# Kernel optimization log

Hardware: AMD Instinct MI355X
Metric: run time of the kernel (lower is better)

The kernel has to match this reference:

```python
import jax, jax.numpy as jnp
import numpy as np

B, P = 8, 768
S = 36                 # sample_points (also deformable offset pairs)
C_IN, C_ADJ = 64, 72   # prior_feat_channels -> adjusted channels
D, G = 512, 4          # fc_hidden_dim, num_groups (= attention heads)
N_OFFSETS, N_STRIPS, DEG = 72, 71, 3


def _bilinear(img, x, y):
    """img: [B,H,W,C]; x,y: [B,N] pixel coords. Bilinear sample, zeros outside."""
    H, W = img.shape[1], img.shape[2]
    x0 = jnp.floor(x); y0 = jnp.floor(y)
    x0i = x0.astype(jnp.int32); y0i = y0.astype(jnp.int32)
    wx1 = x - x0; wy1 = y - y0

    def corner(xi, yi, w):
        valid = (xi >= 0) & (xi < W) & (yi >= 0) & (yi < H)
        xc = jnp.clip(xi, 0, W - 1); yc = jnp.clip(yi, 0, H - 1)
        vals = jax.vmap(lambda f, yy, xx: f[yy, xx])(img, yc, xc)  # [B,N,C]
        return vals * (w * valid)[..., None]

    return (corner(x0i, y0i, (1 - wx1) * (1 - wy1))
            + corner(x0i + 1, y0i, wx1 * (1 - wy1))
            + corner(x0i, y0i + 1, (1 - wx1) * wy1)
            + corner(x0i + 1, y0i + 1, wx1 * wy1))


def _resize_ac(img, Ht, Wt):
    """Bilinear resize with align_corners=True. img: [B,H,W,C]."""
    Bsz, H, W, _ = img.shape
    gy, gx = jnp.meshgrid(jnp.linspace(0.0, H - 1.0, Ht),
                          jnp.linspace(0.0, W - 1.0, Wt), indexing='ij')
    xf = jnp.broadcast_to(gx.reshape(-1), (Bsz, Ht * Wt))
    yf = jnp.broadcast_to(gy.reshape(-1), (Bsz, Ht * Wt))
    return _bilinear(img, xf, yf).reshape(Bsz, Ht, Wt, -1)


def setup_inputs():
    ks = jax.random.split(jax.random.key(0), 32)
    r = lambda i, shp, s=1.0: jax.random.normal(ks[i], shp, dtype=jnp.float32) * s
    z = lambda shp: jnp.zeros(shp, jnp.float32)
    return {
        'feat0': r(0, (B, C_IN, 40, 100)),
        'feat1': r(1, (B, C_IN, 20, 50)),
        'feat2': r(2, (B, C_IN, 10, 25)),
        'priors': jax.random.uniform(ks[3], (B, P, 4 + N_OFFSETS), dtype=jnp.float32) * N_STRIPS,
        'ca_w': r(4, (C_ADJ, C_IN), 0.125), 'ca_b': z((C_ADJ,)),
        'off_w': r(5, (2 * S, C_ADJ), 0.01), 'off_b': r(6, (2 * S,), 0.01),
        'dp_w': r(7, (C_ADJ, C_ADJ), 0.167), 'dp_b': z((C_ADJ,)),
        'z_emb': r(8, (S,), 0.3) + 1.0,
        'gf_w': r(9, (D, S // G, C_ADJ), 0.02), 'gf_b': z((D,)),
        'wq': r(10, (D, D), 0.044), 'bq': z((D,)),
        'wk': r(11, (D, D), 0.044), 'bk': z((D,)),
        'wv': r(12, (D, D), 0.044), 'bv': z((D,)),
        'wo': r(13, (D, D), 0.044), 'bo': z((D,)),
        'cf_w1': r(14, (2 * D, D), 0.044), 'cf_b1': z((2 * D,)),
        'cf_w2': r(15, (D, 2 * D), 0.031), 'cf_b2': z((D,)),
        'cls_w1': r(16, (D, D), 0.044), 'cls_b1': z((D,)),
        'cls_w2': r(17, (2, D), 0.001), 'cls_b2': z((2,)),
        'reg_w1': r(18, (D, D), 0.044), 'reg_b1': z((D,)),
        'p_w1': r(19, (2 * D, D), 0.044), 'p_b1': z((2 * D,)),
        'p_w2': r(20, (DEG + 1, 2 * D), 0.031), 'p_b2': z((DEG + 1,)),
        'b_scale': jnp.ones((1,), jnp.float32), 'b_bias': z((1,)),
    }


def reference(feat0, feat1, feat2, priors, ca_w, ca_b, off_w, off_b, dp_w, dp_b,
              z_emb, gf_w, gf_b, wq, bq, wk, bk, wv, bv, wo, bo,
              cf_w1, cf_b1, cf_w2, cf_b2, cls_w1, cls_b1, cls_w2, cls_b2,
              reg_w1, reg_b1, p_w1, p_b1, p_w2, p_b2, b_scale, b_bias):
    f32 = jnp.float32
    lin = lambda x, w, b: x @ w.T + b

    # ---- prior sampling grid (CLRNet-style) ----
    sx_idx = jnp.floor(jnp.linspace(0.0, 1.0, S) * N_STRIPS).astype(jnp.int32)
    pf_ys = jnp.flip(1.0 - sx_idx.astype(f32) / N_STRIPS)            # [S]
    pf_xs = priors[..., 4 + sx_idx][:, :, ::-1]                       # [B,P,S]
    gx = jnp.clip(pf_xs / N_STRIPS, 0.0, 1.0) * 2.0 - 1.0            # [-1,1]
    gy = jnp.broadcast_to(pf_ys * 2.0 - 1.0, gx.shape)

    # ---- channel adjust (1x1 conv) per level, channels-last ----
    adj = lambda f: jnp.einsum('bchw,oc->bhwo', f, ca_w) + ca_b
    feats = [adj(feat0), adj(feat1), adj(feat2)]                      # [B,H,W,C_ADJ]
    offs0 = jnp.einsum('bhwc,oc->bhwo', feats[0], off_w) + off_b     # [B,H0,W0,2S]

    # ---- deformable multi-level sampling: per (prior, point) gather + 1x1 proj ----
    sidx = jnp.arange(S)
    levels = []
    for l, fl in enumerate(feats):
        Hl, Wl = fl.shape[1], fl.shape[2]
        offs = offs0 if l == 0 else _resize_ac(offs0, Hl, Wl)
        px = (gx + 1.0) * 0.5 * (Wl - 1)
        py = (gy + 1.0) * 0.5 * (Hl - 1)
        ov = _bilinear(offs, px.reshape(B, -1), py.reshape(B, -1)).reshape(B, P, S, S, 2)
        dyx = ov[:, :, sidx, sidx, :]                                 # offset pair s for point s
        sxp = (px + dyx[..., 1]).reshape(B, -1)
        syp = (py + dyx[..., 0]).reshape(B, -1)
        smp = _bilinear(fl, sxp, syp).reshape(B, P, S, C_ADJ)
        levels.append(smp @ dp_w.T + dp_b)
    feat_all = jnp.stack(levels)                                      # [3,B,P,S,C]

    # ---- z-embedding soft level selection ----
    zw = jax.nn.softmax(-(z_emb[:, None] - jnp.arange(3, dtype=f32)) ** 2 / 2.0, axis=-1)  # [S,3]
    feature = jnp.einsum('lbpsc,sl->bpsc', feat_all, zw)

    # ---- grouped gather Conv1d(S -> D, kernel=C_ADJ, groups=G) ----
    xg = feature.reshape(B * P, G, S // G, C_ADJ)
    wg = gf_w.reshape(G, D // G, S // G, C_ADJ)
    feature = (jnp.einsum('ngik,goik->ngo', xg, wg).reshape(B * P, D) + gf_b).reshape(B, P, D)

    # ---- multi-head self-attention over priors + channel MLP residual ----
    dh = D // G
    q = lin(feature, wq, bq).reshape(B, P, G, dh).transpose(0, 2, 1, 3)
    k = lin(feature, wk, bk).reshape(B, P, G, dh).transpose(0, 2, 1, 3)
    v = lin(feature, wv, bv).reshape(B, P, G, dh).transpose(0, 2, 1, 3)
    attn = jax.nn.softmax(jnp.einsum('bgqd,bgkd->bgqk', q, k) / float(np.sqrt(dh)), axis=-1)
    res = jnp.einsum('bgqk,bgkd->bgqd', attn, v).transpose(0, 2, 1, 3).reshape(B, P, D)
    res = lin(res, wo, bo)
    feature = feature + lin(jax.nn.relu(lin(res, cf_w1, cf_b1)), cf_w2, cf_b2)

    # ---- heads ----
    fc = feature.reshape(B * P, D)
    cls_logits = lin(jax.nn.relu(lin(fc, cls_w1, cls_b1)), cls_w2, cls_b2).reshape(B, P, 2)
    reg = jax.nn.relu(lin(fc, reg_w1, reg_b1)).reshape(B, P, D)
    coeffs = lin(jax.nn.relu(lin(reg, p_w1, p_b1)), p_w2, p_b2)       # [B,P,DEG+1]
    coeffs = jnp.concatenate([coeffs[..., :2], coeffs[..., 2:] * b_scale + b_bias], axis=-1)
    ys = jnp.linspace(0.0, 1.0, N_OFFSETS)
    basis = jnp.stack([ys ** i for i in range(DEG + 1)], axis=1)      # [N_OFFSETS, DEG+1]
    xs_pred = jax.nn.sigmoid(jnp.einsum('bnd,od->bno', coeffs, basis))
    return jnp.concatenate([cls_logits, coeffs, xs_pred], axis=-1)    # [B,P,78]
```

## Files before the change

kernel.cpp:

```cpp
#include <hip/hip_runtime.h>
#include <hip/hip_bf16.h>
#include <math.h>

#define BB 8
#define PP 768
#define NPRI 76
#define SS 36
#define CIN 64
#define CADJ 72
#define DD 512

#define H0 40
#define W0 100
#define H1 20
#define W1 50
#define H2 10
#define W2 25

typedef __attribute__((ext_vector_type(8))) short bf16x8;
typedef __attribute__((ext_vector_type(4))) short bf16x4;
typedef __attribute__((ext_vector_type(4))) float f32x4;
#define MFMA_BF16 __builtin_amdgcn_mfma_f32_16x16x32_bf16

typedef const __attribute__((address_space(1))) unsigned int* gas_t;
typedef __attribute__((address_space(3))) unsigned int* las_t;

__device__ __forceinline__ __hip_bfloat16 to_bf16(float v) { return __float2bfloat16(v); }
__device__ __forceinline__ float bf2f(__hip_bfloat16 v) { return __bfloat162float(v); }
__device__ __forceinline__ short to_bf16s(float v) {
    __hip_bfloat16 h = __float2bfloat16(v);
    return *reinterpret_cast<short*>(&h);
}
__device__ __forceinline__ float bfs2f(short s) {
    union { unsigned u; float f; } cv;
    cv.u = ((unsigned)(unsigned short)s) << 16;
    return cv.f;
}

__device__ __forceinline__ float bsample(const float* __restrict__ img, int H, int W,
                                         int C, int c, float x, float y)
{
    float x0f = floorf(x), y0f = floorf(y);
    int x0 = (int)x0f, y0 = (int)y0f;
    float wx1 = x - x0f, wy1 = y - y0f;
    float wx0 = 1.0f - wx1, wy0 = 1.0f - wy1;
    int xc0 = min(max(x0, 0), W - 1);
    int xc1 = min(max(x0 + 1, 0), W - 1);
    int yc0 = min(max(y0, 0), H - 1);
    int yc1 = min(max(y0 + 1, 0), H - 1);
    bool vx0 = (x0 >= 0) && (x0 < W);
    bool vx1 = (x0 + 1 >= 0) && (x0 + 1 < W);
    bool vy0 = (y0 >= 0) && (y0 < H);
    bool vy1 = (y0 + 1 >= 0) && (y0 + 1 < H);
    float w00 = (vx0 && vy0) ? wx0 * wy0 : 0.0f;
    float w01 = (vx1 && vy0) ? wx1 * wy0 : 0.0f;
    float w10 = (vx0 && vy1) ? wx0 * wy1 : 0.0f;
    float w11 = (vx1 && vy1) ? wx1 * wy1 : 0.0f;
    return w00 * img[((size_t)yc0 * W + xc0) * C + c]
         + w01 * img[((size_t)yc0 * W + xc1) * C + c]
         + w10 * img[((size_t)yc1 * W + xc0) * C + c]
         + w11 * img[((size_t)yc1 * W + xc1) * C + c];
}

__device__ __forceinline__ void cast4(__hip_bfloat16* dst, const float* src, long i)
{
    const float4 v = *(const float4*)(src + i * 4);
    bf16x4 pk;
    pk[0] = to_bf16s(v.x); pk[1] = to_bf16s(v.y);
    pk[2] = to_bf16s(v.z); pk[3] = to_bf16s(v.w);
    *(bf16x4*)(dst + i * 4) = pk;
}

__global__ __launch_bounds__(256) void k_wprep(
    const float* __restrict__ wq, const float* __restrict__ wk, const float* __restrict__ wv,
    const float* __restrict__ wo, const float* __restrict__ cf_w1, const float* __restrict__ cf_w2,
    const float* __restrict__ cls_w1, const float* __restrict__ reg_w1, const float* __restrict__ p_w1,
    const float* __restrict__ bq, const float* __restrict__ bk, const float* __restrict__ bv,
    const float* __restrict__ cls_b1, const float* __restrict__ reg_b1,
    const float* __restrict__ gf_w, const float* __restrict__ dp_w,
    const float* __restrict__ dp_b, const float* __restrict__ gf_b,
    __hip_bfloat16* __restrict__ wqkv, __hip_bfloat16* __restrict__ wo_bf,
    __hip_bfloat16* __restrict__ cf1_bf, __hip_bfloat16* __restrict__ cf2_bf,
    __hip_bfloat16* __restrict__ clsreg_bf, __hip_bfloat16* __restrict__ p1_bf,
    __hip_bfloat16* __restrict__ gfw2, float* __restrict__ b2,
    float* __restrict__ bqkv, float* __restrict__ bclsreg)
{
    __shared__ float dpS[CADJ][CADJ + 1];
    __shared__ float gfr[648];
    const int bid = blockIdx.x;
    const int tid = threadIdx.x;

    if (bid < 512) {
        const int o = bid;
        for (int i = tid; i < CADJ * CADJ; i += 256) dpS[i / CADJ][i % CADJ] = dp_w[i];
        for (int i = tid; i < 648; i += 256) gfr[i] = gf_w[(size_t)o * 648 + i];
        __syncthreads();
        for (int t = tid; t < 672; t += 256) {
            float acc = 0.0f;
            if (t < 648) {
                const int i = t / 72, m = t % 72;
                const float* gr = gfr + i * 72;
#pragma unroll 8
                for (int k = 0; k < 72; ++k) acc = fmaf(gr[k], dpS[k][m], acc);
            }
            gfw2[(size_t)o * 672 + t] = to_bf16(acc);
        }
        return;
    }
    if (bid < 514) {
        const int o = (bid - 512) * 256 + tid;
        if (o < DD) {
            const float* gr = gf_w + (size_t)o * 648;
            float acc = gf_b[o];
            for (int j = 0; j < 648; ++j) acc = fmaf(gr[j], dp_b[j % 72], acc);
            b2[o] = acc;
        }
        return;
    }
    if (bid < 3586) {
        long i = (long)(bid - 514) * 256 + tid;
        if (i < 65536) { cast4(wqkv, wq, i); return; }
        i -= 65536;
        if (i < 65536) { cast4(wqkv + 262144, wk, i); return; }
        i -= 65536;
        if (i < 65536) { cast4(wqkv + 524288, wv, i); return; }
        i -= 65536;
        if (i < 65536) { cast4(wo_bf, wo, i); return; }
        i -= 65536;
        if (i < 131072) { cast4(cf1_bf, cf_w1, i); return; }
        i -= 131072;
        if (i < 131072) { cast4(cf2_bf, cf_w2, i); return; }
        i -= 131072;
        if (i < 65536) { cast4(clsreg_bf, cls_w1, i); return; }
        i -= 65536;
        if (i < 65536) { cast4(clsreg_bf + 262144, reg_w1, i); return; }
        i -= 65536;
        if (i < 131072) { cast4(p1_bf, p_w1, i); return; }
        return;
    }
    for (int i = tid; i < 2560; i += 256) {
        if (i < 512) bqkv[i] = bq[i];
        else if (i < 1024) bqkv[i] = bk[i - 512];
        else if (i < 1536) bqkv[i] = bv[i - 1024];
        else if (i < 2048) bclsreg[i - 1536] = cls_b1[i - 1536];
        else bclsreg[i - 1536] = reg_b1[i - 2048];
    }
}

__global__ __launch_bounds__(256) void k_adjoff(
    const float* __restrict__ f, const float* __restrict__ caw, const float* __restrict__ cab,
    const float* __restrict__ offw, const float* __restrict__ offb,
    __hip_bfloat16* __restrict__ feout, float* __restrict__ offout, int HW, int do_off)
{
    __shared__ float inS[64][65];
    __shared__ float wS[72][64];
    __shared__ float owS[72][73];
    __shared__ float feS[64][73];
    __shared__ float cabS[72], obS[72];

    const int tid = threadIdx.x;
    const int b = blockIdx.y;
    const int pix0 = blockIdx.x * 64;
    const int cnt = min(64, HW - pix0);
    const int px = tid & 63, og = tid >> 6, o0 = og * 18;

    const float* fb = f + (size_t)b * CIN * HW + pix0;
    for (int i = tid; i < 72 * 64; i += 256) wS[i >> 6][i & 63] = caw[i];
    if (do_off)
        for (int i = tid; i < 72 * 72; i += 256) owS[i / 72][i % 72] = offw[i];
    if (tid < 72) { cabS[tid] = cab[tid]; obS[tid] = do_off ? offb[tid] : 0.f; }
    for (int i = tid; i < 64 * 64; i += 256) {
        const int c = i >> 6, p = i & 63;
        inS[c][p] = (p < cnt) ? fb[(size_t)c * HW + p] : 0.f;
    }
    __syncthreads();

    float acc[18];
#pragma unroll
    for (int j = 0; j < 18; ++j) acc[j] = cabS[o0 + j];
#pragma unroll 4
    for (int c = 0; c < 64; ++c) {
        const float v = inS[c][px];
#pragma unroll
        for (int j = 0; j < 18; ++j) acc[j] = fmaf(v, wS[o0 + j][c], acc[j]);
    }
#pragma unroll
    for (int j = 0; j < 18; ++j) feS[px][o0 + j] = acc[j];
    __syncthreads();

    __hip_bfloat16* feg = feout + ((size_t)b * HW + pix0) * CADJ;
    for (int i = tid; i < cnt * CADJ; i += 256) feg[i] = to_bf16(feS[i / CADJ][i % CADJ]);

    if (!do_off) return;

    float acc2[18];
#pragma unroll
    for (int j = 0; j < 18; ++j) acc2[j] = obS[o0 + j];
#pragma unroll 4
    for (int c = 0; c < 72; ++c) {
        const float v = feS[px][c];
#pragma unroll
        for (int j = 0; j < 18; ++j) acc2[j] = fmaf(v, owS[o0 + j][c], acc2[j]);
    }
    __syncthreads();
#pragma unroll
    for (int j = 0; j < 18; ++j) feS[px][o0 + j] = acc2[j];
    __syncthreads();
    float* ofg = offout + ((size_t)b * HW + pix0) * CADJ;
    for (int i = tid; i < cnt * CADJ; i += 256) ofg[i] = feS[i / CADJ][i % CADJ];
}

__global__ __launch_bounds__(256) void k_adjr12(
    const float* __restrict__ f1, const float* __restrict__ f2,
    const float* __restrict__ caw, const float* __restrict__ cab,
    __hip_bfloat16* __restrict__ fe1, __hip_bfloat16* __restrict__ fe2,
    const float* __restrict__ of0, float* __restrict__ of1, float* __restrict__ of2)
{
    const int blk = blockIdx.x;
    const int tid = threadIdx.x;

    if (blk < 160) {
        __shared__ float inS[64][65];
        __shared__ float wS[72][64];
        __shared__ float feS[64][73];
        __shared__ float cabS[72];

        const int bx = blk % 20;
        const int b = blk / 20;
        const float* f;
        __hip_bfloat16* fe;
        int HW, pix0;
        if (bx < 16) { f = f1; fe = fe1; HW = H1 * W1; pix0 = bx * 64; }
        else         { f = f2; fe = fe2; HW = H2 * W2; pix0 = (bx - 16) * 64; }
        const int cnt = min(64, HW - pix0);
        const int px = tid & 63, og = tid >> 6, o0 = og * 18;

        const float* fb = f + (size_t)b * CIN * HW + pix0;
        for (int i = tid; i < 72 * 64; i += 256) wS[i >> 6][i & 63] = caw[i];
        if (tid < 72) cabS[tid] = cab[tid];
        for (int i = tid; i < 64 * 64; i += 256) {
            const int c = i >> 6, p = i & 63;
            inS[c][p] = (p < cnt) ? fb[(size_t)c * HW + p] : 0.f;
        }
        __syncthreads();

        float acc[18];
#pragma unroll
        for (int j = 0; j < 18; ++j) acc[j] = cabS[o0 + j];
#pragma unroll 4
        for (int c = 0; c < 64; ++c) {
            const float v = inS[c][px];
#pragma unroll
            for (int j = 0; j < 18; ++j) acc[j] = fmaf(v, wS[o0 + j][c], acc[j]);
        }
#pragma unroll
        for (int j = 0; j < 18; ++j) feS[px][o0 + j] = acc[j];
        __syncthreads();

        __hip_bfloat16* feg = fe + ((size_t)b * HW + pix0) * CADJ;
        for (int i = tid; i < cnt * CADJ; i += 256) feg[i] = to_bf16(feS[i / CADJ][i % CADJ]);
        return;
    }

    const int T1 = BB * H1 * W1 * CADJ;
    const int T2 = BB * H2 * W2 * CADJ;
    int idx = (blk - 160) * 256 + tid;
    if (idx < T1) {
        const int c = idx % CADJ;
        const int j = (idx / CADJ) % W1;
        const int i = (idx / (CADJ * W1)) % H1;
        const int b = idx / (CADJ * W1 * H1);
        float sy = fminf((float)i * ((float)(H0 - 1) / (float)(H1 - 1)), (float)(H0 - 1));
        float sx = fminf((float)j * ((float)(W0 - 1) / (float)(W1 - 1)), (float)(W0 - 1));
        of1[idx] = bsample(of0 + (size_t)b * H0 * W0 * CADJ, H0, W0, CADJ, c, sx, sy);
        return;
    }
    idx -= T1;
    if (idx >= T2) return;
    const int c = idx % CADJ;
    const int j = (idx / CADJ) % W2;
    const int i = (idx / (CADJ * W2)) % H2;
    const int b = idx / (CADJ * W2 * H2);
    float sy = fminf((float)i * ((float)(H0 - 1) / (float)(H2 - 1)), (float)(H0 - 1));
    float sx = fminf((float)j * ((float)(W0 - 1) / (float)(W2 - 1)), (float)(W0 - 1));
    of2[idx] = bsample(of0 + (size_t)b * H0 * W0 * CADJ, H0, W0, CADJ, c, sx, sy);
}

__global__ __launch_bounds__(256) void k_sample(
    const float* __restrict__ priors,
    const __hip_bfloat16* __restrict__ feats0, const __hip_bfloat16* __restrict__ feats1,
    const __hip_bfloat16* __restrict__ feats2,
    const float* __restrict__ offs0,  const float* __restrict__ offs1,  const float* __restrict__ offs2,
    const float* __restrict__ z_emb,
    __hip_bfloat16* __restrict__ fsout)
{
    const int bid = blockIdx.x;
    const int gi = (bid & 7) * 384 + (bid >> 3);
    const int bp0 = gi * 2;
    const int b = bp0 / PP;
    const int tid = threadIdx.x;

    __shared__ __align__(16) int   ib[2][3][SS][4];
    __shared__ __align__(16) float wz[2][3][SS][4];

    const int Hs[3] = {H0, H1, H2};
    const int Wsz[3] = {W0, W1, W2};
    const __hip_bfloat16* Fb[3] = { feats0 + (size_t)b * H0 * W0 * CADJ,
                                    feats1 + (size_t)b * H1 * W1 * CADJ,
                                    feats2 + (size_t)b * H2 * W2 * CADJ };
    const float* Ob[3] = { offs0 + (size_t)b * H0 * W0 * CADJ,
                           offs1 + (size_t)b * H1 * W1 * CADJ,
                           offs2 + (size_t)b * H2 * W2 * CADJ };

    if (tid < 2 * 3 * SS) {
        const int p = tid / 108;
        const int l = (tid % 108) / SS;
        const int s = tid % SS;
        const int bp = bp0 + p;
        const float t = (float)(35 - s) / 35.0f;
        const int m = (int)floorf(t * 71.0f);
        const float pfx = priors[(size_t)bp * NPRI + 4 + m];
        const float gxv = fminf(fmaxf(pfx / 71.0f, 0.0f), 1.0f) * 2.0f - 1.0f;
        const float gyv = (1.0f - (float)m / 71.0f) * 2.0f - 1.0f;
        const float z = z_emb[s];
        const float e0 = expf(-0.5f * z * z);
        const float e1 = expf(-0.5f * (z - 1.0f) * (z - 1.0f));
        const float e2 = expf(-0.5f * (z - 2.0f) * (z - 2.0f));
        const float inv = 1.0f / (e0 + e1 + e2);
        const float ev[3] = {e0, e1, e2};
        const float zwl = ev[l] * inv;

        const int Hl = Hs[l], Wl = Wsz[l];
        const float px = (gxv + 1.0f) * 0.5f * (float)(Wl - 1);
        const float py = (gyv + 1.0f) * 0.5f * (float)(Hl - 1);
        const float dy = bsample(Ob[l], Hl, Wl, CADJ, 2 * s,     px, py);
        const float dx = bsample(Ob[l], Hl, Wl, CADJ, 2 * s + 1, px, py);
        const float sx = px + dx, sy = py + dy;
        const float x0f = floorf(sx), y0f = floorf(sy);
        const int x0 = (int)x0f, y0 = (int)y0f;
        const float wx1 = sx - x0f, wy1 = sy - y0f;
        const float wx0 = 1.0f - wx1, wy0 = 1.0f - wy1;
        const bool vx0 = (x0 >= 0) && (x0 < Wl);
        const bool vx1 = (x0 + 1 >= 0) && (x0 + 1 < Wl);
        const bool vy0 = (y0 >= 0) && (y0 < Hl);
        const bool vy1 = (y0 + 1 >= 0) && (y0 + 1 < Hl);
        const int xc0 = min(max(x0, 0), Wl - 1);
        const int xc1 = min(max(x0 + 1, 0), Wl - 1);
        const int yc0 = min(max(y0, 0), Hl - 1);
        const int yc1 = min(max(y0 + 1, 0), Hl - 1);
        wz[p][l][s][0] = ((vx0 && vy0) ? wx0 * wy0 : 0.0f) * zwl;
        wz[p][l][s][1] = ((vx1 && vy0) ? wx1 * wy0 : 0.0f) * zwl;
        wz[p][l][s][2] = ((vx0 && vy1) ? wx0 * wy1 : 0.0f) * zwl;
        wz[p][l][s][3] = ((vx1 && vy1) ? wx1 * wy1 : 0.0f) * zwl;
        ib[p][l][s][0] = (yc0 * Wl + xc0) * CADJ;
        ib[p][l][s][1] = (yc0 * Wl + xc1) * CADJ;
        ib[p][l][s][2] = (yc1 * Wl + xc0) * CADJ;
        ib[p][l][s][3] = (yc1 * Wl + xc1) * CADJ;
    }
    __syncthreads();

    for (int idx = tid; idx < SS * 18; idx += 256) {
        const int s = idx / 18, k4 = (idx % 18) * 4;
        float a[2][4] = {{0.f, 0.f, 0.f, 0.f}, {0.f, 0.f, 0.f, 0.f}};
#pragma unroll
        for (int p = 0; p < 2; ++p)
#pragma unroll
            for (int l = 0; l < 3; ++l) {
                const __hip_bfloat16* F = Fb[l];
                const int4   i4 = *(const int4*)&ib[p][l][s][0];
                const float4 w4 = *(const float4*)&wz[p][l][s][0];
                const bf16x4 v0 = *(const bf16x4*)(F + i4.x + k4);
                const bf16x4 v1 = *(const bf16x4*)(F + i4.y + k4);
                const bf16x4 v2 = *(const bf16x4*)(F + i4.z + k4);
                const bf16x4 v3 = *(const bf16x4*)(F + i4.w + k4);
                a[p][0] = fmaf(w4.x, bfs2f(v0[0]), a[p][0]);
                a[p][1] = fmaf(w4.x, bfs2f(v0[1]), a[p][1]);
                a[p][2] = fmaf(w4.x, bfs2f(v0[2]), a[p][2]);
                a[p][3] = fmaf(w4.x, bfs2f(v0[3]), a[p][3]);
                a[p][0] = fmaf(w4.y, bfs2f(v1[0]), a[p][0]);
                a[p][1] = fmaf(w4.y, bfs2f(v1[1]), a[p][1]);
                a[p][2] = fmaf(w4.y, bfs2f(v1[2]), a[p][2]);
                a[p][3] = fmaf(w4.y, bfs2f(v1[3]), a[p][3]);
                a[p][0] = fmaf(w4.z, bfs2f(v2[0]), a[p][0]);
                a[p][1] = fmaf(w4.z, bfs2f(v2[1]), a[p][1]);
                a[p][2] = fmaf(w4.z, bfs2f(v2[2]), a[p][2]);
                a[p][3] = fmaf(w4.z, bfs2f(v2[3]), a[p][3]);
                a[p][0] = fmaf(w4.w, bfs2f(v3[0]), a[p][0]);
                a[p][1] = fmaf(w4.w, bfs2f(v3[1]), a[p][1]);
                a[p][2] = fmaf(w4.w, bfs2f(v3[2]), a[p][2]);
                a[p][3] = fmaf(w4.w, bfs2f(v3[3]), a[p][3]);
            }
        const int col = (s / 9) * 672 + (s % 9) * 72 + k4;
#pragma unroll
        for (int p = 0; p < 2; ++p) {
            bf16x4 pk;
            pk[0] = to_bf16s(a[p][0]); pk[1] = to_bf16s(a[p][1]);
            pk[2] = to_bf16s(a[p][2]); pk[3] = to_bf16s(a[p][3]);
            *(bf16x4*)&fsout[(size_t)(bp0 + p) * 2688 + col] = pk;
        }
    }
    if (tid < 2 * 96) {
        const int p = tid / 96, g = (tid % 96) / 24, t = tid % 24;
        fsout[(size_t)(bp0 + p) * 2688 + g * 672 + 648 + t] = to_bf16(0.0f);
    }
}

__global__ __launch_bounds__(256) void k_bgemm(
    const __hip_bfloat16* __restrict__ A, int lda, long sAz,
    const __hip_bfloat16* __restrict__ W, int ldw, long sWz,
    const float* __restrict__ bias, int sBz,
    const __hip_bfloat16* __restrict__ Res, int ldres,
    __hip_bfloat16* __restrict__ C, int ldc, int sCz,
    int K, int relu)
{
    __shared__ __hip_bfloat16 As[2][128][32];
    __shared__ __hip_bfloat16 Bs[2][128][32];
    const int tid = threadIdx.x;
    const int lane = tid & 63, w = tid >> 6;
    const int wr = w >> 1, wc = w & 1;
    const int row16 = lane & 15, kg = lane >> 4;
    const int z = blockIdx.z;
    const int m0 = blockIdx.y * 128, n0 = blockIdx.x * 128;
    const __hip_bfloat16* Ab = A + (size_t)z * sAz;
    const __hip_bfloat16* Wb = W + (size_t)z * sWz;
    const int gr = lane >> 2;
    const int gc = (lane & 3) * 8;

#define STAGE128(buf, kbase)                                                       \
    {                                                                              \
        _Pragma("unroll")                                                          \
        for (int c = 0; c < 2; ++c) {                                              \
            const int r = w * 32 + c * 16;                                         \
            __builtin_amdgcn_global_load_lds(                                      \
                (gas_t)(Ab + (size_t)(m0 + r + gr) * lda + (kbase) + gc),          \
                (las_t)&As[buf][r][0], 16, 0, 0);                                  \
            __builtin_amdgcn_global_load_lds(                                      \
                (gas_t)(Wb + (size_t)(n0 + r + gr) * ldw + (kbase) + gc),          \
                (las_t)&Bs[buf][r][0], 16, 0, 0);                                  \
        }                                                                          \
    }

    f32x4 acc[4][4];
#pragma unroll
    for (int i = 0; i < 4; ++i)
#pragma unroll
        for (int j = 0; j < 4; ++j) acc[i][j] = (f32x4){0.f, 0.f, 0.f, 0.f};

    STAGE128(0, 0)
    __syncthreads();

    int cur = 0;
    for (int k0 = 0; k0 < K; k0 += 32) {
        if (k0 + 32 < K) STAGE128(cur ^ 1, k0 + 32)
        bf16x8 af[4], bfr[4];
#pragma unroll
        for (int i = 0; i < 4; ++i) af[i]  = *(const bf16x8*)&As[cur][wr * 64 + i * 16 + row16][kg * 8];
#pragma unroll
        for (int j = 0; j < 4; ++j) bfr[j] = *(const bf16x8*)&Bs[cur][wc * 64 + j * 16 + row16][kg * 8];
#pragma unroll
        for (int i = 0; i < 4; ++i)
#pragma unroll
            for (int j = 0; j < 4; ++j)
                acc[i][j] = MFMA_BF16(af[i], bfr[j], acc[i][j], 0, 0, 0);
        __syncthreads();
        cur ^= 1;
    }
#undef STAGE128

    const float* bz = bias + (size_t)z * sBz;
    __hip_bfloat16* Cz = C + (size_t)z * sCz;
#pragma unroll
    for (int i = 0; i < 4; ++i) {
#pragma unroll
        for (int r = 0; r < 4; ++r) {
            const int row = m0 + wr * 64 + i * 16 + kg * 4 + r;
#pragma unroll
            for (int j = 0; j < 4; ++j) {
                const int col = n0 + wc * 64 + j * 16 + row16;
                float v = acc[i][j][r] + bz[col];
                if (Res) v += bf2f(Res[(size_t)row * ldres + col]);
                if (relu) v = fmaxf(v, 0.0f);
                Cz[(size_t)row * ldc + col] = to_bf16(v);
            }
        }
    }
}

__global__ __launch_bounds__(256) void k_bgemm64(
    const __hip_bfloat16* __restrict__ A, int lda, long sAz,
    const __hip_bfloat16* __restrict__ W, int ldw, long sWz,
    const float* __restrict__ bias, int sBz,
    const __hip_bfloat16* __restrict__ Res, int ldres,
    __hip_bfloat16* __restrict__ C, int ldc, int sCz,
    int K, int relu)
{
    __shared__ __hip_bfloat16 As[2][64][32];
    __shared__ __hip_bfloat16 Bs[2][64][32];
    const int tid = threadIdx.x;
    const int lane = tid & 63, w = tid >> 6;
    const int wr = w >> 1, wc = w & 1;
    const int row16 = lane & 15, kg = lane >> 4;
    const int z = blockIdx.z;
    const int m0 = blockIdx.y * 64, n0 = blockIdx.x * 64;
    const __hip_bfloat16* Ab = A + (size_t)z * sAz;
    const __hip_bfloat16* Wb = W + (size_t)z * sWz;
    const int gr = lane >> 2;
    const int gc = (lane & 3) * 8;

    f32x4 acc[2][2];
#pragma unroll
    for (int i = 0; i < 2; ++i)
#pragma unroll
        for (int j = 0; j < 2; ++j) acc[i][j] = (f32x4){0.f, 0.f, 0.f, 0.f};

    __builtin_amdgcn_global_load_lds(
        (gas_t)(Ab + (size_t)(m0 + w * 16 + gr) * lda + gc),
        (las_t)&As[0][w * 16][0], 16, 0, 0);
    __builtin_amdgcn_global_load_lds(
        (gas_t)(Wb + (size_t)(n0 + w * 16 + gr) * ldw + gc),
        (las_t)&Bs[0][w * 16][0], 16, 0, 0);
    __syncthreads();

    int cur = 0;
    for (int k0 = 0; k0 < K; k0 += 32) {
        if (k0 + 32 < K) {
            const int nxt = cur ^ 1;
            __builtin_amdgcn_global_load_lds(
                (gas_t)(Ab + (size_t)(m0 + w * 16 + gr) * lda + k0 + 32 + gc),
                (las_t)&As[nxt][w * 16][0], 16, 0, 0);
            __builtin_amdgcn_global_load_lds(
                (gas_t)(Wb + (size_t)(n0 + w * 16 + gr) * ldw + k0 + 32 + gc),
                (las_t)&Bs[nxt][w * 16][0], 16, 0, 0);
        }
        bf16x8 af[2], bfr[2];
#pragma unroll
        for (int i = 0; i < 2; ++i) af[i]  = *(const bf16x8*)&As[cur][wr * 32 + i * 16 + row16][kg * 8];
#pragma unroll
        for (int j = 0; j < 2; ++j) bfr[j] = *(const bf16x8*)&Bs[cur][wc * 32 + j * 16 + row16][kg * 8];
#pragma unroll
        for (int i = 0; i < 2; ++i)
#pragma unroll
            for (int j = 0; j < 2; ++j)
                acc[i][j] = MFMA_BF16(af[i], bfr[j], acc[i][j], 0, 0, 0);
        __syncthreads();
        cur ^= 1;
    }

    const float* bz = bias + (size_t)z * sBz;
    __hip_bfloat16* Cz = C + (size_t)z * sCz;
#pragma unroll
    for (int i = 0; i < 2; ++i) {
#pragma unroll
        for (int r = 0; r < 4; ++r) {
            const int row = m0 + wr * 32 + i * 16 + kg * 4 + r;
#pragma unroll
            for (int j = 0; j < 2; ++j) {
                const int col = n0 + wc * 32 + j * 16 + row16;
                float v = acc[i][j][r] + bz[col];
                if (Res) v += bf2f(Res[(size_t)row * ldres + col]);
                if (relu) v = fmaxf(v, 0.0f);
                Cz[(size_t)row * ldc + col] = to_bf16(v);
            }
        }
    }
}

__global__ __launch_bounds__(256) void k_vt(
    const __hip_bfloat16* __restrict__ qkv, __hip_bfloat16* __restrict__ Vt)
{
    const int kt = blockIdx.x;
    const int bg = blockIdx.y;
    const int b = bg >> 2, g = bg & 3;
    const int tid = threadIdx.x;
    __shared__ unsigned short Vs[64][130];

    const __hip_bfloat16* src = qkv + (size_t)(b * PP + kt * 64) * 1536 + 1024 + g * 128;
    for (int i = tid; i < 1024; i += 256) {
        const int row = i >> 4, ch = i & 15;
        *(bf16x8*)&Vs[row][ch * 8] = *(const bf16x8*)(src + (size_t)row * 1536 + ch * 8);
    }
    __syncthreads();
    __hip_bfloat16* dst = Vt + (size_t)bg * 128 * 768 + kt * 64;
    for (int i = tid; i < 1024; i += 256) {
        const int d = i >> 3, kc = i & 7;
        bf16x8 pk;
#pragma unroll
        for (int j = 0; j < 8; ++j) pk[j] = (short)Vs[kc * 8 + j][d];
        *(bf16x8*)(dst + (size_t)d * 768 + kc * 8) = pk;
    }
}

__global__ __launch_bounds__(256) void k_fattn(
    const __hip_bfloat16* __restrict__ qkv, const __hip_bfloat16* __restrict__ Vt,
    __hip_bfloat16* __restrict__ Out)
{
    const int id = blockIdx.x;
    const int xcd = id & 7, rest = id >> 3;
    const int bg = xcd * 4 + rest / 12;
    const int qt = rest % 12;
    const int b = bg >> 2, g = bg & 3;
    const int tid = threadIdx.x, lane = tid & 63, w = tid >> 6;
    const int row16 = lane & 15, kg = lane >> 4;
    const int q0 = qt * 64;

    __shared__ __hip_bfloat16 Klds[64][136];
    __shared__ __hip_bfloat16 Vtl[128][72];
    __shared__ __hip_bfloat16 Plds[4][16][72];

    const size_t rowQ = (size_t)(b * PP + q0 + w * 16 + row16) * 1536 + g * 128;
    bf16x8 aq[4];
#pragma unroll
    for (int t = 0; t < 4; ++t)
        aq[t] = *(const bf16x8*)(qkv + rowQ + t * 32 + kg * 8);

    f32x4 oacc[8];
#pragma unroll
    for (int dt = 0; dt < 8; ++dt) oacc[dt] = (f32x4){0.f, 0.f, 0.f, 0.f};
    float mrow[4] = {-3.0e38f, -3.0e38f, -3.0e38f, -3.0e38f};
    float lrow[4] = {0.f, 0.f, 0.f, 0.f};

    const __hip_bfloat16* Kb = qkv + (size_t)(b * PP) * 1536 + 512 + g * 128;
    const __hip_bfloat16* Vb = Vt + (size_t)bg * 128 * 768;
    const float sc = 0.08838834764831845f;

    const int krow = tid >> 2, kch = tid & 3;
    const int vrow = tid >> 1, vch = tid & 1;
    bf16x8 kreg[4], vreg[4];

    {
        const __hip_bfloat16* s1 = Kb + (size_t)krow * 1536 + kch * 32;
        const __hip_bfloat16* s2 = Vb + (size_t)vrow * 768 + vch * 32;
#pragma unroll
        for (int j = 0; j < 4; ++j) { kreg[j] = *(const bf16x8*)(s1 + j * 8);
                                      vreg[j] = *(const bf16x8*)(s2 + j * 8); }
    }

    for (int kt = 0; kt < 12; ++kt) {
        __syncthreads();
#pragma unroll
        for (int j = 0; j < 4; ++j) {
            *(bf16x8*)&Klds[krow][kch * 32 + j * 8] = kreg[j];
            *(bf16x8*)&Vtl[vrow][vch * 32 + j * 8] = vreg[j];
        }
        __syncthreads();
        if (kt < 11) {
            const __hip_bfloat16* s1 = Kb + (size_t)((kt + 1) * 64 + krow) * 1536 + kch * 32;
            const __hip_bfloat16* s2 = Vb + (size_t)vrow * 768 + (kt + 1) * 64 + vch * 32;
#pragma unroll
            for (int j = 0; j < 4; ++j) { kreg[j] = *(const bf16x8*)(s1 + j * 8);
                                          vreg[j] = *(const bf16x8*)(s2 + j * 8); }
        }

        f32x4 s4[4];
#pragma unroll
        for (int st = 0; st < 4; ++st) s4[st] = (f32x4){0.f, 0.f, 0.f, 0.f};
        __builtin_amdgcn_s_setprio(1);
#pragma unroll
        for (int st = 0; st < 4; ++st)
#pragma unroll
            for (int t = 0; t < 4; ++t)
                s4[st] = MFMA_BF16(aq[t],
                    *(const bf16x8*)&Klds[st * 16 + row16][t * 32 + kg * 8], s4[st], 0, 0, 0);
        __builtin_amdgcn_s_setprio(0);

        float pm[4];
#pragma unroll
        for (int r = 0; r < 4; ++r) {
            float m0 = fmaxf(fmaxf(s4[0][r], s4[1][r]), fmaxf(s4[2][r], s4[3][r])) * sc;
            m0 = fmaxf(m0, __shfl_xor(m0, 1));
            m0 = fmaxf(m0, __shfl_xor(m0, 2));
            m0 = fmaxf(m0, __shfl_xor(m0, 4));
            m0 = fmaxf(m0, __shfl_xor(m0, 8));
            pm[r] = m0;
        }
        const float need = fmaxf(fmaxf(pm[0] - mrow[0], pm[1] - mrow[1]),
                                 fmaxf(pm[2] - mrow[2], pm[3] - mrow[3]));
        if (!__all(need <= 8.0f)) {
#pragma unroll
            for (int r = 0; r < 4; ++r) {
                const float mn = fmaxf(mrow[r], pm[r]);
                const float so = __expf(mrow[r] - mn);
                lrow[r] *= so;
#pragma unroll
                for (int dt = 0; dt < 8; ++dt) oacc[dt][r] *= so;
                mrow[r] = mn;
            }
        }
#pragma unroll
        for (int r = 0; r < 4; ++r) {
            float rs = 0.f;
#pragma unroll
            for (int st = 0; st < 4; ++st) {
                const float p = __expf(s4[st][r] * sc - mrow[r]);
                rs += p;
                Plds[w][kg * 4 + r][st * 16 + row16] = to_bf16(p);
            }
            rs += __shfl_xor(rs, 1);
            rs += __shfl_xor(rs, 2);
            rs += __shfl_xor(rs, 4);
            rs += __shfl_xor(rs, 8);
            lrow[r] += rs;
        }

        __builtin_amdgcn_s_setprio(1);
#pragma unroll
        for (int ks = 0; ks < 2; ++ks) {
            bf16x8 ap = *(const bf16x8*)&Plds[w][row16][ks * 32 + kg * 8];
#pragma unroll
            for (int dt = 0; dt < 8; ++dt)
                oacc[dt] = MFMA_BF16(ap,
                    *(const bf16x8*)&Vtl[dt * 16 + row16][ks * 32 + kg * 8], oacc[dt], 0, 0, 0);
        }
        __builtin_amdgcn_s_setprio(0);
    }

    const size_t obase = (size_t)(b * PP + q0 + w * 16 + kg * 4) * DD + g * 128;
#pragma unroll
    for (int r = 0; r < 4; ++r) {
        const float inv = 1.0f / lrow[r];
#pragma unroll
        for (int dt = 0; dt < 8; ++dt)
            Out[obase + (size_t)r * DD + dt * 16 + row16] = to_bf16(oacc[dt][r] * inv);
    }
}

__global__ __launch_bounds__(256) void k_head(
    const __hip_bfloat16* __restrict__ clsreg, const __hip_bfloat16* __restrict__ ph,
    const float* __restrict__ cls_w2, const float* __restrict__ cls_b2,
    const float* __restrict__ p_w2, const float* __restrict__ p_b2,
    const float* __restrict__ b_scale, const float* __restrict__ b_bias,
    float* __restrict__ outp)
{
    const int bp = blockIdx.x * 4 + (threadIdx.x >> 6);
    const int lane = threadIdx.x & 63;
    const __hip_bfloat16* hr = clsreg + (size_t)bp * 1024;
    float a0 = 0.0f, a1 = 0.0f;
    for (int i = lane; i < DD; i += 64) {
        float h = bf2f(hr[i]);
        a0 = fmaf(h, cls_w2[i], a0);
        a1 = fmaf(h, cls_w2[DD + i], a1);
    }
    const __hip_bfloat16* pr = ph + (size_t)bp * 1024;
    float c0 = 0.0f, c1 = 0.0f, c2 = 0.0f, c3 = 0.0f;
    for (int i = lane; i < 1024; i += 64) {
        float h = bf2f(pr[i]);
        c0 = fmaf(h, p_w2[i], c0);
        c1 = fmaf(h, p_w2[1024 + i], c1);
        c2 = fmaf(h, p_w2[2048 + i], c2);
        c3 = fmaf(h, p_w2[3072 + i], c3);
    }
#pragma unroll
    for (int off = 32; off > 0; off >>= 1) {
        a0 += __shfl_down(a0, off);
        a1 += __shfl_down(a1, off);
        c0 += __shfl_down(c0, off);
        c1 += __shfl_down(c1, off);
        c2 += __shfl_down(c2, off);
        c3 += __shfl_down(c3, off);
    }
    a0 = __shfl(a0, 0); a1 = __shfl(a1, 0);
    c0 = __shfl(c0, 0); c1 = __shfl(c1, 0);
    c2 = __shfl(c2, 0); c3 = __shfl(c3, 0);
    const float k0 = c0 + p_b2[0];
    const float k1 = c1 + p_b2[1];
    const float scv = b_scale[0], biv = b_bias[0];
    const float k2 = (c2 + p_b2[2]) * scv + biv;
    const float k3 = (c3 + p_b2[3]) * scv + biv;
    float* orow = outp + (size_t)bp * 78;
    if (lane == 0) {
        orow[0] = a0 + cls_b2[0];
        orow[1] = a1 + cls_b2[1];
        orow[2] = k0; orow[3] = k1; orow[4] = k2; orow[5] = k3;
    }
    for (int o = lane; o < 72; o += 64) {
        float ys = (float)o / 71.0f;
        float tv = k0 + ys * (k1 + ys * (k2 + ys * k3));
        orow[6 + o] = 1.0f / (1.0f + expf(-tv));
    }
}

extern "C" void kernel_launch(void* const* d_in, const int* in_sizes, int n_in,
                              void* d_out, int out_size, void* d_ws, size_t ws_size,
                              hipStream_t stream)
{
    const float* feat0  = (const float*)d_in[0];
    const float* feat1  = (const float*)d_in[1];
    const float* feat2  = (const float*)d_in[2];
    const float* priors = (const float*)d_in[3];
    const float* ca_w   = (const float*)d_in[4];
    const float* ca_b   = (const float*)d_in[5];
    const float* off_w  = (const float*)d_in[6];
    const float* off_b  = (const float*)d_in[7];
    const float* dp_w   = (const float*)d_in[8];
    const float* dp_b   = (const float*)d_in[9];
    const float* z_emb  = (const float*)d_in[10];
    const float* gf_w   = (const float*)d_in[11];
    const float* gf_b   = (const float*)d_in[12];
    const float* wq     = (const float*)d_in[13];
    const float* bq     = (const float*)d_in[14];
    const float* wk     = (const float*)d_in[15];
    const float* bk     = (const float*)d_in[16];
    const float* wv     = (const float*)d_in[17];
    const float* bv     = (const float*)d_in[18];
    const float* wo     = (const float*)d_in[19];
    const float* bo     = (const float*)d_in[20];
    const float* cf_w1  = (const float*)d_in[21];
    const float* cf_b1  = (const float*)d_in[22];
    const float* cf_w2  = (const float*)d_in[23];
    const float* cf_b2  = (const float*)d_in[24];
    const float* cls_w1 = (const float*)d_in[25];
    const float* cls_b1 = (const float*)d_in[26];
    const float* cls_w2 = (const float*)d_in[27];
    const float* cls_b2 = (const float*)d_in[28];
    const float* reg_w1 = (const float*)d_in[29];
    const float* reg_b1 = (const float*)d_in[30];
    const float* p_w1   = (const float*)d_in[31];
    const float* p_b1   = (const float*)d_in[32];
    const float* p_w2   = (const float*)d_in[33];
    const float* p_b2   = (const float*)d_in[34];
    const float* b_scale = (const float*)d_in[35];
    const float* b_bias  = (const float*)d_in[36];
    float* out = (float*)d_out;

    char* wsb = (char*)d_ws;
    __hip_bfloat16* feature = (__hip_bfloat16*)(wsb + 0);
    __hip_bfloat16* qkvb    = (__hip_bfloat16*)(wsb + 6291456);
    __hip_bfloat16* tb      = (__hip_bfloat16*)(wsb + 25165824);
    __hip_bfloat16* vtb     = (__hip_bfloat16*)(wsb + 31457280);
    __hip_bfloat16* rb      = (__hip_bfloat16*)(wsb + 31457280);
    __hip_bfloat16* hb      = (__hip_bfloat16*)(wsb + 37748736);
    __hip_bfloat16* f2      = (__hip_bfloat16*)(wsb + 50331648);
    __hip_bfloat16* clsregb = (__hip_bfloat16*)(wsb + 56623104);
    __hip_bfloat16* phb     = (__hip_bfloat16*)(wsb + 69206016);
    float* of1 = (float*)(wsb + 6291456);
    float* of2 = (float*)(wsb + 8595456);
    __hip_bfloat16* fe1 = (__hip_bfloat16*)(wsb + 9171456);
    __hip_bfloat16* fe2 = (__hip_bfloat16*)(wsb + 11475456);
    __hip_bfloat16* fsb = (__hip_bfloat16*)(wsb + 25165824);
    __hip_bfloat16* fe0 = (__hip_bfloat16*)(wsb + 58195968);
    float* of0 = (float*)(wsb + 67411968);
    __hip_bfloat16* wqkv_bf   = (__hip_bfloat16*)(wsb + 81788928);
    __hip_bfloat16* wo_bf     = (__hip_bfloat16*)(wsb + 83361792);
    __hip_bfloat16* cf1_bf    = (__hip_bfloat16*)(wsb + 83886080);
    __hip_bfloat16* cf2_bf    = (__hip_bfloat16*)(wsb + 84934656);
    __hip_bfloat16* clsreg_bf = (__hip_bfloat16*)(wsb + 85983232);
    __hip_bfloat16* p1_bf     = (__hip_bfloat16*)(wsb + 87031808);
    __hip_bfloat16* gfw2_bf   = (__hip_bfloat16*)(wsb + 88080384);
    float* bqkv    = (float*)(wsb + 88768512);
    float* bclsreg = (float*)(wsb + 88774656);
    float* b2      = (float*)(wsb + 88778752);

    k_wprep<<<3587, 256, 0, stream>>>(
        wq, wk, wv, wo, cf_w1, cf_w2, cls_w1, reg_w1, p_w1, bq, bk, bv, cls_b1, reg_b1,
        gf_w, dp_w, dp_b, gf_b,
        wqkv_bf, wo_bf, cf1_bf, cf2_bf, clsreg_bf, p1_bf, gfw2_bf, b2, bqkv, bclsreg);

    k_adjoff<<<dim3(63, BB), 256, 0, stream>>>(feat0, ca_w, ca_b, off_w, off_b,
                                               fe0, of0, H0 * W0, 1);
    k_adjr12<<<160 + (BB * (H1 * W1 + H2 * W2) * CADJ + 255) / 256, 256, 0, stream>>>(
        feat1, feat2, ca_w, ca_b, fe1, fe2, of0, of1, of2);
    k_sample<<<3072, 256, 0, stream>>>(priors, fe0, fe1, fe2, of0, of1, of2, z_emb, fsb);

    const int M = BB * PP;
    k_bgemm64<<<dim3(2, M / 64, 4), 256, 0, stream>>>(
        fsb, 2688, 672, gfw2_bf, 672, 128 * 672, b2, 128,
        nullptr, 0, feature, DD, 128, 672, 0);
    k_bgemm<<<dim3(12, M / 128, 1), 256, 0, stream>>>(
        feature, DD, 0, wqkv_bf, DD, 0, bqkv, 0,
        nullptr, 0, qkvb, 1536, 0, DD, 0);
    k_vt<<<dim3(12, 32), 256, 0, stream>>>(qkvb, vtb);
    k_fattn<<<384, 256, 0, stream>>>(qkvb, vtb, tb);
    k_bgemm64<<<dim3(8, M / 64, 1), 256, 0, stream>>>(
        tb, DD, 0, wo_bf, DD, 0, bo, 0, nullptr, 0, rb, DD, 0, DD, 0);
    k_bgemm64<<<dim3(16, M / 64, 1), 256, 0, stream>>>(
        rb, DD, 0, cf1_bf, DD, 0, cf_b1, 0, nullptr, 0, hb, 1024, 0, DD, 1);
    k_bgemm64<<<dim3(8, M / 64, 1), 256, 0, stream>>>(
        hb, 1024, 0, cf2_bf, 1024, 0, cf_b2, 0, feature, DD, f2, DD, 0, 1024, 0);
    k_bgemm64<<<dim3(16, M / 64, 1), 256, 0, stream>>>(
        f2, DD, 0, clsreg_bf, DD, 0, bclsreg, 0, nullptr, 0, clsregb, 1024, 0, DD, 1);
    k_bgemm64<<<dim3(16, M / 64, 1), 256, 0, stream>>>(
        clsregb + 512, 1024, 0, p1_bf, DD, 0, p_b1, 0, nullptr, 0, phb, 1024, 0, DD, 1);

    k_head<<<M / 4, 256, 0, stream>>>(clsregb, phb, cls_w2, cls_b2, p_w2, p_b2, b_scale, b_bias, out);
}
```

Before: 285.2 us.

## Split flash attention into 32-query tiles and flatten sampling loop over priors

The flash-attention kernel now uses 128-thread blocks with two waves, each block covering 32 queries, and launches twice as many blocks (768) so more of the GPU's compute units are busy. Each thread now stages twice as many K/V registers per tile. K and V tiles are loaded once per 32 queries instead of once per 64, which doubles global and LDS traffic for K/V. The sampling kernel's gather loop now spreads both priors across threads rather than having each thread loop over them, which gives more parallel work per block and fewer live accumulators per thread.

```diff
diff --git a/kernel.cpp b/kernel.cpp
--- a/kernel.cpp
+++ b/kernel.cpp
@@ -359,45 +359,34 @@
     }
     __syncthreads();
 
-    for (int idx = tid; idx < SS * 18; idx += 256) {
-        const int s = idx / 18, k4 = (idx % 18) * 4;
-        float a[2][4] = {{0.f, 0.f, 0.f, 0.f}, {0.f, 0.f, 0.f, 0.f}};
-#pragma unroll
-        for (int p = 0; p < 2; ++p)
-#pragma unroll
-            for (int l = 0; l < 3; ++l) {
-                const __hip_bfloat16* F = Fb[l];
-                const int4   i4 = *(const int4*)&ib[p][l][s][0];
-                const float4 w4 = *(const float4*)&wz[p][l][s][0];
-                const bf16x4 v0 = *(const bf16x4*)(F + i4.x + k4);
-                const bf16x4 v1 = *(const bf16x4*)(F + i4.y + k4);
-                const bf16x4 v2 = *(const bf16x4*)(F + i4.z + k4);
-                const bf16x4 v3 = *(const bf16x4*)(F + i4.w + k4);
-                a[p][0] = fmaf(w4.x, bfs2f(v0[0]), a[p][0]);
-                a[p][1] = fmaf(w4.x, bfs2f(v0[1]), a[p][1]);
-                a[p][2] = fmaf(w4.x, bfs2f(v0[2]), a[p][2]);
-                a[p][3] = fmaf(w4.x, bfs2f(v0[3]), a[p][3]);
-                a[p][0] = fmaf(w4.y, bfs2f(v1[0]), a[p][0]);
-                a[p][1] = fmaf(w4.y, bfs2f(v1[1]), a[p][1]);
-                a[p][2] = fmaf(w4.y, bfs2f(v1[2]), a[p][2]);
-                a[p][3] = fmaf(w4.y, bfs2f(v1[3]), a[p][3]);
-                a[p][0] = fmaf(w4.z, bfs2f(v2[0]), a[p][0]);
-                a[p][1] = fmaf(w4.z, bfs2f(v2[1]), a[p][1]);
-                a[p][2] = fmaf(w4.z, bfs2f(v2[2]), a[p][2]);
-                a[p][3] = fmaf(w4.z, bfs2f(v2[3]), a[p][3]);
-                a[p][0] = fmaf(w4.w, bfs2f(v3[0]), a[p][0]);
-                a[p][1] = fmaf(w4.w, bfs2f(v3[1]), a[p][1]);
-                a[p][2] = fmaf(w4.w, bfs2f(v3[2]), a[p][2]);
-                a[p][3] = fmaf(w4.w, bfs2f(v3[3]), a[p][3]);
-            }
-        const int col = (s / 9) * 672 + (s % 9) * 72 + k4;
-#pragma unroll
-        for (int p = 0; p < 2; ++p) {
-            bf16x4 pk;
-            pk[0] = to_bf16s(a[p][0]); pk[1] = to_bf16s(a[p][1]);
-            pk[2] = to_bf16s(a[p][2]); pk[3] = to_bf16s(a[p][3]);
-            *(bf16x4*)&fsout[(size_t)(bp0 + p) * 2688 + col] = pk;
-        }
+    for (int idx = tid; idx < 2 * SS * 18; idx += 256) {
+        const int p = idx / 648;
+        const int rem = idx % 648;
+        const int s = rem / 18, k4 = (rem % 18) * 4;
+        float a0 = 0.f, a1 = 0.f, a2 = 0.f, a3 = 0.f;
+#pragma unroll
+        for (int l = 0; l < 3; ++l) {
+            const __hip_bfloat16* F = Fb[l];
+            const int4   i4 = *(const int4*)&ib[p][l][s][0];
+            const float4 w4 = *(const float4*)&wz[p][l][s][0];
+            const bf16x4 v0 = *(const bf16x4*)(F + i4.x + k4);
+            const bf16x4 v1 = *(const bf16x4*)(F + i4.y + k4);
+            const bf16x4 v2 = *(const bf16x4*)(F + i4.z + k4);
+            const bf16x4 v3 = *(const bf16x4*)(F + i4.w + k4);
+            a0 = fmaf(w4.x, bfs2f(v0[0]), a0); a1 = fmaf(w4.x, bfs2f(v0[1]), a1);
+            a2 = fmaf(w4.x, bfs2f(v0[2]), a2); a3 = fmaf(w4.x, bfs2f(v0[3]), a3);
+            a0 = fmaf(w4.y, bfs2f(v1[0]), a0); a1 = fmaf(w4.y, bfs2f(v1[1]), a1);
+            a2 = fmaf(w4.y, bfs2f(v1[2]), a2); a3 = fmaf(w4.y, bfs2f(v1[3]), a3);
+            a0 = fmaf(w4.z, bfs2f(v2[0]), a0); a1 = fmaf(w4.z, bfs2f(v2[1]), a1);
+            a2 = fmaf(w4.z, bfs2f(v2[2]), a2); a3 = fmaf(w4.z, bfs2f(v2[3]), a3);
+            a0 = fmaf(w4.w, bfs2f(v3[0]), a0); a1 = fmaf(w4.w, bfs2f(v3[1]), a1);
+            a2 = fmaf(w4.w, bfs2f(v3[2]), a2); a3 = fmaf(w4.w, bfs2f(v3[3]), a3);
+        }
+        bf16x4 pk;
+        pk[0] = to_bf16s(a0); pk[1] = to_bf16s(a1);
+        pk[2] = to_bf16s(a2); pk[3] = to_bf16s(a3);
+        __hip_bfloat16* orow = fsout + (size_t)(bp0 + p) * 2688;
+        *(bf16x4*)&orow[(s / 9) * 672 + (s % 9) * 72 + k4] = pk;
     }
     if (tid < 2 * 96) {
         const int p = tid / 96, g = (tid % 96) / 24, t = tid % 24;
@@ -590,22 +579,22 @@
     }
 }
 
-__global__ __launch_bounds__(256) void k_fattn(
+__global__ __launch_bounds__(128) void k_fattn(
     const __hip_bfloat16* __restrict__ qkv, const __hip_bfloat16* __restrict__ Vt,
     __hip_bfloat16* __restrict__ Out)
 {
     const int id = blockIdx.x;
     const int xcd = id & 7, rest = id >> 3;
-    const int bg = xcd * 4 + rest / 12;
-    const int qt = rest % 12;
+    const int bg = xcd * 4 + rest / 24;
+    const int qt = rest % 24;
     const int b = bg >> 2, g = bg & 3;
     const int tid = threadIdx.x, lane = tid & 63, w = tid >> 6;
     const int row16 = lane & 15, kg = lane >> 4;
-    const int q0 = qt * 64;
+    const int q0 = qt * 32;
 
     __shared__ __hip_bfloat16 Klds[64][136];
     __shared__ __hip_bfloat16 Vtl[128][72];
-    __shared__ __hip_bfloat16 Plds[4][16][72];
+    __shared__ __hip_bfloat16 Plds[2][16][72];
 
     const size_t rowQ = (size_t)(b * PP + q0 + w * 16 + row16) * 1536 + g * 128;
     bf16x8 aq[4];
@@ -623,31 +612,30 @@
     const __hip_bfloat16* Vb = Vt + (size_t)bg * 128 * 768;
     const float sc = 0.08838834764831845f;
 
-    const int krow = tid >> 2, kch = tid & 3;
-    const int vrow = tid >> 1, vch = tid & 1;
-    bf16x8 kreg[4], vreg[4];
+    const int krow = tid >> 1, kch = tid & 1;
+    bf16x8 kreg[8], vreg[8];
 
     {
-        const __hip_bfloat16* s1 = Kb + (size_t)krow * 1536 + kch * 32;
-        const __hip_bfloat16* s2 = Vb + (size_t)vrow * 768 + vch * 32;
-#pragma unroll
-        for (int j = 0; j < 4; ++j) { kreg[j] = *(const bf16x8*)(s1 + j * 8);
+        const __hip_bfloat16* s1 = Kb + (size_t)krow * 1536 + kch * 64;
+        const __hip_bfloat16* s2 = Vb + (size_t)tid * 768;
+#pragma unroll
+        for (int j = 0; j < 8; ++j) { kreg[j] = *(const bf16x8*)(s1 + j * 8);
                                       vreg[j] = *(const bf16x8*)(s2 + j * 8); }
     }
 
     for (int kt = 0; kt < 12; ++kt) {
         __syncthreads();
 #pragma unroll
-        for (int j = 0; j < 4; ++j) {
-            *(bf16x8*)&Klds[krow][kch * 32 + j * 8] = kreg[j];
-            *(bf16x8*)&Vtl[vrow][vch * 32 + j * 8] = vreg[j];
+        for (int j = 0; j < 8; ++j) {
+            *(bf16x8*)&Klds[krow][kch * 64 + j * 8] = kreg[j];
+            *(bf16x8*)&Vtl[tid][j * 8] = vreg[j];
         }
         __syncthreads();
         if (kt < 11) {
-            const __hip_bfloat16* s1 = Kb + (size_t)((kt + 1) * 64 + krow) * 1536 + kch * 32;
-            const __hip_bfloat16* s2 = Vb + (size_t)vrow * 768 + (kt + 1) * 64 + vch * 32;
-#pragma unroll
-            for (int j = 0; j < 4; ++j) { kreg[j] = *(const bf16x8*)(s1 + j * 8);
+            const __hip_bfloat16* s1 = Kb + (size_t)((kt + 1) * 64 + krow) * 1536 + kch * 64;
+            const __hip_bfloat16* s2 = Vb + (size_t)tid * 768 + (kt + 1) * 64;
+#pragma unroll
+            for (int j = 0; j < 8; ++j) { kreg[j] = *(const bf16x8*)(s1 + j * 8);
                                           vreg[j] = *(const bf16x8*)(s2 + j * 8); }
         }
 
@@ -869,7 +857,7 @@
         feature, DD, 0, wqkv_bf, DD, 0, bqkv, 0,
         nullptr, 0, qkvb, 1536, 0, DD, 0);
     k_vt<<<dim3(12, 32), 256, 0, stream>>>(qkvb, vtb);
-    k_fattn<<<384, 256, 0, stream>>>(qkvb, vtb, tb);
+    k_fattn<<<768, 128, 0, stream>>>(qkvb, vtb, tb);
     k_bgemm64<<<dim3(8, M / 64, 1), 256, 0, stream>>>(
         tb, DD, 0, wo_bf, DD, 0, bo, 0, nullptr, 0, rb, DD, 0, DD, 0);
     k_bgemm64<<<dim3(16, M / 64, 1), 256, 0, stream>>>(
```

New measurement: 289.3 us. No clear change (+1.4%).
